# Kernel tuning notes

Measured on AMD Instinct MI355X. Metric: run time of the kernel, lower is better.

## Reference

```python
import jax, jax.numpy as jnp
import numpy as np
from jax import lax

D_MODEL, D_INNER, N_STATE, DT_RANK, K = 1024, 2048, 16, 64, 3
B_SZ, SEQ = 2, 1024

def silu(v):
    return v * jax.nn.sigmoid(v)

def setup_inputs() -> dict:
    key = jax.random.key(0)
    ks = jax.random.split(key, 12)
    s = 0.02
    return {
        'x': jax.random.normal(ks[0], (B_SZ, SEQ, D_MODEL), jnp.float32),
        'A_log': jax.random.normal(ks[1], (D_INNER, N_STATE), jnp.float32) * 0.5,
        'W_in': jax.random.normal(ks[2], (D_MODEL, 2 * D_INNER), jnp.float32) * s,
        'b_in': jax.random.normal(ks[3], (2 * D_INNER,), jnp.float32) * s,
        'conv_w': jax.random.normal(ks[4], (D_INNER, 1, K), jnp.float32) * s,  # depthwise [O,I/g,K]
        'conv_b': jax.random.normal(ks[5], (D_INNER,), jnp.float32) * s,
        'W_x': jax.random.normal(ks[6], (D_INNER, DT_RANK + 2 * N_STATE), jnp.float32) * s,
        'W_dt': jax.random.normal(ks[7], (DT_RANK, D_INNER), jnp.float32) * s,
        'b_dt': jax.random.normal(ks[8], (D_INNER,), jnp.float32) * s,
        'W_out': jax.random.normal(ks[9], (D_INNER, D_MODEL), jnp.float32) * s,
        'b_out': jax.random.normal(ks[10], (D_MODEL,), jnp.float32) * s,
    }

def selective_scan(u, delta, A, B, C):
    # u, delta: [b,l,d]; A: [d,n]; B, C: [b,l,n]
    deltaA = jnp.exp(jnp.einsum('bld,dn->bldn', delta, A))          # [b,l,d,n]
    deltaBu = jnp.einsum('bld,bln,bld->bldn', delta, B, u)           # [b,l,d,n]
    h0 = jnp.zeros((u.shape[0], u.shape[2], A.shape[1]), u.dtype)    # [b,d,n]
    def step(h, inp):
        dA_t, dBu_t, C_t = inp
        h = dA_t * h + dBu_t
        y = jnp.einsum('bdn,bn->bd', h, C_t)
        return h, y
    xs = (jnp.moveaxis(deltaA, 1, 0), jnp.moveaxis(deltaBu, 1, 0), jnp.moveaxis(C, 1, 0))
    _, ys = lax.scan(step, h0, xs)                                   # [l,b,d]
    return jnp.moveaxis(ys, 0, 1)                                    # [b,l,d]

def reference(x, A_log, W_in, b_in, conv_w, conv_b, W_x, W_dt, b_dt, W_out, b_out):
    xr = x @ W_in + b_in                                             # [b,l,2*d_inner]
    u, res = jnp.split(xr, 2, axis=-1)
    # causal depthwise conv1d (pad left k-1, truncate == torch pad=k-1 then slice)
    uc = lax.conv_general_dilated(
        jnp.moveaxis(u, 1, 2), conv_w, window_strides=(1,),
        padding=[(K - 1, 0)], feature_group_count=D_INNER,
        dimension_numbers=('NCH', 'OIH', 'NCH'))
    u = silu(jnp.moveaxis(uc, 2, 1) + conv_b)                        # [b,l,d_inner]
    xp = u @ W_x                                                     # [b,l,dt_rank+2n]
    dt, Bm, Cm = jnp.split(xp, [DT_RANK, DT_RANK + N_STATE], axis=-1)
    delta = jax.nn.softplus(dt @ W_dt + b_dt)                        # [b,l,d_inner]
    A = -jnp.exp(A_log)                                              # [d_inner,n]
    y = selective_scan(u, delta, A, Bm, Cm)                          # [b,l,d_inner]
    y = y * silu(res)
    return y @ W_out + b_out
```

## Files before the change

### kernel.cpp

```cpp
#include <hip/hip_runtime.h>

#define D_MODEL 1024
#define D_INNER 2048
#define N_ST    16
#define DT_RANK 64
#define BSZ     2
#define SEQL    1024
#define NTOK    (BSZ*SEQL)
#define NC      32
#define LC      (SEQL/NC)

typedef __attribute__((ext_vector_type(4))) float f32x4;
typedef __attribute__((ext_vector_type(8))) short bf16x8;

__device__ __forceinline__ short f2b(float f) {
  unsigned u = __builtin_bit_cast(unsigned, f);
  u += 0x7fffu + ((u >> 16) & 1u);
  return (short)(u >> 16);
}

__device__ __forceinline__ float b2f(unsigned short s) {
  return __builtin_bit_cast(float, (unsigned)s << 16);
}

__device__ __forceinline__ void gload16(const void* g, void* l) {
  __builtin_amdgcn_global_load_lds(
      (const __attribute__((address_space(1))) void*)g,
      (__attribute__((address_space(3))) void*)l, 16, 0, 0);
}

template<int SOFTPLUS, int PARTIAL, int RESSPLIT, int OUTB16, int FIXUP>
__global__ __launch_bounds__(256)
void gemm_kernel(const short* __restrict__ A, const short* __restrict__ Bm,
                 const float* __restrict__ bias, float* __restrict__ C,
                 short* __restrict__ upb, short* __restrict__ resb,
                 const float* __restrict__ cw, const float* __restrict__ cb,
                 short* __restrict__ ubuf,
                 int M, int N, int K, int lda, int ldb, int ldc, int kChunk)
{
  __shared__ short sA[2][128 * 64];
  __shared__ short sB[2][128 * 64];
  const int tid  = threadIdx.x;
  const int lane = tid & 63;
  const int wave = tid >> 6;
  const int wr = wave >> 1, wc = wave & 1;
  const int lr = lane & 15, lg = lane >> 4;

  int bx = blockIdx.x, by = blockIdx.y;
  if (RESSPLIT) {
    const int lin = by * 32 + bx;
    const int lb = (lin & 7) * 64 + (lin >> 3);
    bx = lb >> 4; by = lb & 15;
  }
  const int m0 = by * 128;
  const int n0 = bx * 128;
  const int kStart = blockIdx.z * kChunk;
  int kEnd = kStart + kChunk; if (kEnd > K) kEnd = K;
  const int nt = (kEnd - kStart) >> 6;

  if (FIXUP) {
    const int tt = m0 + (tid >> 7);
    const int dd = kStart + (tid & 127);
    const int l  = tt & (SEQL - 1);
    float u2 = b2f((unsigned short)upb[(size_t)tt * 2048 + dd]);
    float u1 = (l >= 1) ? b2f((unsigned short)upb[(size_t)(tt - 1) * 2048 + dd]) : 0.f;
    float u0 = (l >= 2) ? b2f((unsigned short)upb[(size_t)(tt - 2) * 2048 + dd]) : 0.f;
    float r = cb[dd] + cw[dd * 3] * u0 + cw[dd * 3 + 1] * u1 + cw[dd * 3 + 2] * u2;
    ubuf[(size_t)tt * 2048 + dd] = f2b(r / (1.f + __expf(-r)));
    asm volatile("s_waitcnt vmcnt(0)" ::: "memory");
    __syncthreads();
  }

  const int srow = lane >> 3;
  const int scol = ((lane & 7) ^ srow) * 8;
  const short* aS = A + (size_t)(m0 + wave * 32 + srow) * lda + scol + kStart;
  const short* bS = Bm + (size_t)(n0 + wave * 32 + srow) * ldb + scol + kStart;
  const int ldsOff = wave * 2048;

#define STAGE(buf, koff)                                                   \
  {                                                                        \
    _Pragma("unroll")                                                      \
    for (int i_ = 0; i_ < 4; ++i_) {                                       \
      gload16(aS + (size_t)(i_ * 8) * lda + (koff), &sA[buf][ldsOff + i_ * 512]); \
      gload16(bS + (size_t)(i_ * 8) * ldb + (koff), &sB[buf][ldsOff + i_ * 512]); \
    }                                                                      \
  }

  f32x4 acc[4][4];
#pragma unroll
  for (int i = 0; i < 4; ++i)
#pragma unroll
    for (int j = 0; j < 4; ++j) acc[i][j] = (f32x4){0.f, 0.f, 0.f, 0.f};

  STAGE(0, 0);

  for (int t = 0; t < nt; ++t) {
    const int cur = t & 1;
    if (t + 1 < nt) {
      STAGE(cur ^ 1, (t + 1) * 64);
      asm volatile("s_waitcnt vmcnt(8)" ::: "memory");
    } else {
      asm volatile("s_waitcnt vmcnt(0)" ::: "memory");
    }
    __builtin_amdgcn_s_barrier();

#pragma unroll
    for (int kk = 0; kk < 2; ++kk) {
      bf16x8 aF[4], bF[4];
#pragma unroll
      for (int mi = 0; mi < 4; ++mi) {
        const int row = wr * 64 + mi * 16 + lr;
        aF[mi] = *reinterpret_cast<const bf16x8*>(
            &sA[cur][row * 64 + (((kk * 4 + lg) ^ (lr & 7)) * 8)]);
      }
#pragma unroll
      for (int ni = 0; ni < 4; ++ni) {
        const int row = wc * 64 + ni * 16 + lr;
        bF[ni] = *reinterpret_cast<const bf16x8*>(
            &sB[cur][row * 64 + (((kk * 4 + lg) ^ (lr & 7)) * 8)]);
      }
#pragma unroll
      for (int mi = 0; mi < 4; ++mi)
#pragma unroll
        for (int ni = 0; ni < 4; ++ni)
          acc[mi][ni] = __builtin_amdgcn_mfma_f32_16x16x32_bf16(
              aF[mi], bF[ni], acc[mi][ni], 0, 0, 0);
    }
    __builtin_amdgcn_s_barrier();
  }
#undef STAGE

  if (RESSPLIT) {
    if (n0 < 2048) {
      short (*sU)[128] = reinterpret_cast<short (*)[128]>(&sA[0][0]);
#pragma unroll
      for (int mi = 0; mi < 4; ++mi) {
#pragma unroll
        for (int ni = 0; ni < 4; ++ni) {
          const int cl = wc * 64 + ni * 16 + lr;
          const float bv = bias[n0 + cl];
#pragma unroll
          for (int j = 0; j < 4; ++j) {
            const int rl = wr * 64 + mi * 16 + lg * 4 + j;
            const short s = f2b(acc[mi][ni][j] + bv);
            sU[rl][cl] = s;
            if (rl < 2 || rl >= 126)
              upb[(size_t)(m0 + rl) * 2048 + (n0 + cl)] = s;
          }
        }
      }
      __syncthreads();
#pragma unroll
      for (int ni = 0; ni < 4; ++ni) {
        const int cl = wc * 64 + ni * 16 + lr;
        const int col = n0 + cl;
        const float w0 = cw[col * 3], w1 = cw[col * 3 + 1], w2 = cw[col * 3 + 2];
        const float cbv = cb[col];
#pragma unroll
        for (int mi = 0; mi < 4; ++mi) {
#pragma unroll
          for (int j = 0; j < 4; ++j) {
            const int rl = wr * 64 + mi * 16 + lg * 4 + j;
            if (rl >= 2) {
              float r = cbv + w0 * b2f((unsigned short)sU[rl - 2][cl])
                            + w1 * b2f((unsigned short)sU[rl - 1][cl])
                            + w2 * b2f((unsigned short)sU[rl][cl]);
              ubuf[(size_t)(m0 + rl) * 2048 + col] = f2b(r / (1.f + __expf(-r)));
            }
          }
        }
      }
    } else {
#pragma unroll
      for (int mi = 0; mi < 4; ++mi) {
        const int row = m0 + wr * 64 + mi * 16 + lg * 4;
#pragma unroll
        for (int ni = 0; ni < 4; ++ni) {
          const int col = n0 + wc * 64 + ni * 16 + lr;
          const float bv = bias[col];
#pragma unroll
          for (int j = 0; j < 4; ++j) {
            float v = acc[mi][ni][j] + bv;
            resb[(size_t)(row + j) * 2048 + (col - 2048)] =
                f2b(v / (1.f + __expf(-v)));
          }
        }
      }
    }
    return;
  }

#pragma unroll
  for (int mi = 0; mi < 4; ++mi) {
    const int row = m0 + wr * 64 + mi * 16 + lg * 4;
#pragma unroll
    for (int ni = 0; ni < 4; ++ni) {
      const int col = n0 + wc * 64 + ni * 16 + lr;
      if (OUTB16) {
        const float bv = bias[col];
#pragma unroll
        for (int j = 0; j < 4; ++j) {
          float v = acc[mi][ni][j] + bv;
          if (SOFTPLUS) v = fmaxf(v, 0.f) + log1pf(__expf(-fabsf(v)));
          upb[(size_t)(row + j) * ldc + col] = f2b(v);
        }
      } else if (PARTIAL == 2) {
        short* Cs = (short*)C + (size_t)blockIdx.z * M * ldc;
#pragma unroll
        for (int j = 0; j < 4; ++j)
          Cs[(size_t)(row + j) * ldc + col] = f2b(acc[mi][ni][j]);
      } else if (col < N) {
        float* Cp = PARTIAL ? C + (size_t)blockIdx.z * M * ldc : C;
        float bv = (bias != nullptr && blockIdx.z == 0) ? bias[col] : 0.f;
#pragma unroll
        for (int j = 0; j < 4; ++j) {
          float v = acc[mi][ni][j] + bv;
          if (SOFTPLUS) v = fmaxf(v, 0.f) + log1pf(__expf(-fabsf(v)));
          Cp[(size_t)(row + j) * ldc + col] = v;
        }
      }
    }
  }
}

__device__ __forceinline__ void trans_body(const float* __restrict__ in,
                                           short* __restrict__ out,
                                           int R, int C, int bx, int by,
                                           short (*t)[33], int tidx)
{
  const int c0 = bx * 32, r0 = by * 32;
  const int cc = tidx & 31, rr = tidx >> 5;
#pragma unroll
  for (int i = 0; i < 4; ++i)
    t[rr + i * 8][cc] = f2b(in[(size_t)(r0 + rr + i * 8) * C + c0 + cc]);
  __syncthreads();
#pragma unroll
  for (int i = 0; i < 4; ++i)
    out[(size_t)(c0 + rr + i * 8) * R + r0 + cc] = t[cc][rr + i * 8];
}

#define PB_CAST  2048
#define PB_WIN   4096
#define PB_WX    192
#define PB_WDT   128
#define PB_WOUT  2048

__global__ __launch_bounds__(256)
void prep_kernel(const float* __restrict__ x,    const float* __restrict__ W_in,
                 const float* __restrict__ W_x,  const float* __restrict__ W_dt,
                 const float* __restrict__ W_out,
                 short* __restrict__ xb,  short* __restrict__ Wib,
                 short* __restrict__ Wxb, short* __restrict__ Wdtb,
                 short* __restrict__ Wob)
{
  __shared__ short t[32][33];
  const int bid = blockIdx.x, tidx = threadIdx.x;
  if (bid < PB_CAST) {
    const int i = bid * 256 + tidx;
    float4 v = *reinterpret_cast<const float4*>(x + (size_t)i * 4);
    *reinterpret_cast<short4*>(xb + (size_t)i * 4) =
        make_short4(f2b(v.x), f2b(v.y), f2b(v.z), f2b(v.w));
  } else if (bid < PB_CAST + PB_WIN) {
    const int b = bid - PB_CAST;
    trans_body(W_in, Wib, 1024, 4096, b % 128, b / 128, t, tidx);
  } else if (bid < PB_CAST + PB_WIN + PB_WX) {
    const int b = bid - PB_CAST - PB_WIN;
    trans_body(W_x, Wxb, 2048, 96, b % 3, b / 3, t, tidx);
  } else if (bid < PB_CAST + PB_WIN + PB_WX + PB_WDT) {
    const int b = bid - PB_CAST - PB_WIN - PB_WX;
    trans_body(W_dt, Wdtb, 64, 2048, b % 64, b / 64, t, tidx);
  } else {
    const int b = bid - PB_CAST - PB_WIN - PB_WX - PB_WDT;
    trans_body(W_out, Wob, 2048, 1024, b % 32, b / 32, t, tidx);
  }
}

__global__ __launch_bounds__(256)
void combine16_kernel(const float* __restrict__ part, float* __restrict__ xp,
                      short* __restrict__ dtb)
{
  const int gid = blockIdx.x * 256 + threadIdx.x;
  const int r = gid / 24, q = gid - r * 24;
  float4 s = make_float4(0.f, 0.f, 0.f, 0.f);
#pragma unroll
  for (int c = 0; c < 16; ++c) {
    const float4 v = *reinterpret_cast<const float4*>(
        part + (size_t)c * 2048 * 96 + (size_t)r * 96 + q * 4);
    s.x += v.x; s.y += v.y; s.z += v.z; s.w += v.w;
  }
  *reinterpret_cast<float4*>(xp + (size_t)r * 96 + q * 4) = s;
  if (q < 16)
    *reinterpret_cast<short4*>(dtb + (size_t)r * 64 + q * 4) =
        make_short4(f2b(s.x), f2b(s.y), f2b(s.z), f2b(s.w));
}

__global__ __launch_bounds__(256)
void combine4_kernel(const unsigned short* __restrict__ part,
                     const float* __restrict__ bias, float* __restrict__ out)
{
  const int gid = blockIdx.x * 256 + threadIdx.x;
  const int r = gid >> 8, c4 = gid & 255;
  const float4 bv = *reinterpret_cast<const float4*>(bias + c4 * 4);
  float4 s = bv;
#pragma unroll
  for (int z = 0; z < 4; ++z) {
    const ushort4 v = *reinterpret_cast<const ushort4*>(
        part + (size_t)z * 2048 * 1024 + (size_t)r * 1024 + c4 * 4);
    s.x += b2f(v.x); s.y += b2f(v.y); s.z += b2f(v.z); s.w += b2f(v.w);
  }
  *reinterpret_cast<float4*>(out + (size_t)r * 1024 + c4 * 4) = s;
}

__global__ __launch_bounds__(256, 4)
void scan_pass1(const unsigned short* __restrict__ deltab, const unsigned short* __restrict__ ub,
                const float* __restrict__ xp, const float* __restrict__ A_log,
                float* __restrict__ sdl, float* __restrict__ HS)
{
  const int d = blockIdx.y * 256 + threadIdx.x;
  const int c = blockIdx.x, b = blockIdx.z;
  const int t0 = (b << 10) + c * LC;
  float Ac[16];
#pragma unroll
  for (int q = 0; q < 4; ++q) {
    float4 a = *reinterpret_cast<const float4*>(A_log + (size_t)d * 16 + q * 4);
    Ac[q * 4 + 0] = -__expf(a.x); Ac[q * 4 + 1] = -__expf(a.y);
    Ac[q * 4 + 2] = -__expf(a.z); Ac[q * 4 + 3] = -__expf(a.w);
  }
  float h[16];
#pragma unroll
  for (int n = 0; n < 16; ++n) h[n] = 0.f;
  float sd = 0.f;
  const unsigned short* dp = deltab + (size_t)t0 * 2048 + d;
  const unsigned short* up = ub + (size_t)t0 * 2048 + d;
  const float* xb = xp + (size_t)t0 * 96 + DT_RANK;
#pragma unroll 4
  for (int t = 0; t < LC; ++t) {
    float dl = b2f(dp[(size_t)t * 2048]);
    float ul = b2f(up[(size_t)t * 2048]);
    float Bf[16];
#pragma unroll
    for (int q = 0; q < 4; ++q)
      *reinterpret_cast<float4*>(&Bf[q * 4]) =
          *reinterpret_cast<const float4*>(xb + (size_t)t * 96 + q * 4);
    float dlu = dl * ul;
    sd += dl;
#pragma unroll
    for (int n = 0; n < 16; ++n)
      h[n] = __expf(dl * Ac[n]) * h[n] + dlu * Bf[n];
  }
  sdl[((size_t)b * NC + c) * 2048 + d] = sd;
  float* hs = HS + (((size_t)b * NC + c) * 2048 + d) * 16;
#pragma unroll
  for (int q = 0; q < 4; ++q)
    *reinterpret_cast<float4*>(hs + q * 4) =
        make_float4(h[q * 4], h[q * 4 + 1], h[q * 4 + 2], h[q * 4 + 3]);
}

__global__ __launch_bounds__(256)
void scan_pass2(const float* __restrict__ sdl, const float* __restrict__ A_log,
                float* __restrict__ HS)
{
  const int gid = blockIdx.x * 256 + threadIdx.x;
  const int b = gid >> 15, rest = gid & 32767;
  const int d = rest >> 4;
  const float Ac = -__expf(A_log[rest]);
  float P[NC], S[NC];
#pragma unroll
  for (int c = 0; c < NC; ++c)
    P[c] = sdl[(((size_t)b * NC + c) << 11) + d];
#pragma unroll
  for (int c = 0; c < NC; ++c)
    S[c] = HS[(((size_t)b * NC + c) << 15) + rest];
#pragma unroll
  for (int c = 0; c < NC; ++c)
    P[c] = __expf(P[c] * Ac);
  float h = 0.f;
#pragma unroll
  for (int c = 0; c < NC; ++c) {
    HS[(((size_t)b * NC + c) << 15) + rest] = h;
    h = P[c] * h + S[c];
  }
}

__global__ __launch_bounds__(256, 4)
void scan_pass3(const unsigned short* __restrict__ deltab, const unsigned short* __restrict__ ub,
                const float* __restrict__ xp, const float* __restrict__ A_log,
                const float* __restrict__ HS, const unsigned short* __restrict__ rb,
                short* __restrict__ zb)
{
  const int d = blockIdx.y * 256 + threadIdx.x;
  const int c = blockIdx.x, b = blockIdx.z;
  const int t0 = (b << 10) + c * LC;
  float Ac[16];
#pragma unroll
  for (int q = 0; q < 4; ++q) {
    float4 a = *reinterpret_cast<const float4*>(A_log + (size_t)d * 16 + q * 4);
    Ac[q * 4 + 0] = -__expf(a.x); Ac[q * 4 + 1] = -__expf(a.y);
    Ac[q * 4 + 2] = -__expf(a.z); Ac[q * 4 + 3] = -__expf(a.w);
  }
  float h[16];
  const float* hs = HS + (((size_t)b * NC + c) * 2048 + d) * 16;
#pragma unroll
  for (int q = 0; q < 4; ++q) {
    float4 v = *reinterpret_cast<const float4*>(hs + q * 4);
    h[q * 4 + 0] = v.x; h[q * 4 + 1] = v.y; h[q * 4 + 2] = v.z; h[q * 4 + 3] = v.w;
  }
  const unsigned short* dp = deltab + (size_t)t0 * 2048 + d;
  const unsigned short* up = ub + (size_t)t0 * 2048 + d;
  const float* xb = xp + (size_t)t0 * 96 + DT_RANK;
  const float* xc = xp + (size_t)t0 * 96 + DT_RANK + N_ST;
  const unsigned short* rp = rb + (size_t)t0 * 2048 + d;
  short* zp = zb + (size_t)t0 * 2048 + d;
#pragma unroll 4
  for (int t = 0; t < LC; ++t) {
    float dl = b2f(dp[(size_t)t * 2048]);
    float ul = b2f(up[(size_t)t * 2048]);
    float rv = b2f(rp[(size_t)t * 2048]);
    float Bf[16], Cf[16];
#pragma unroll
    for (int q = 0; q < 4; ++q) {
      *reinterpret_cast<float4*>(&Bf[q * 4]) =
          *reinterpret_cast<const float4*>(xb + (size_t)t * 96 + q * 4);
      *reinterpret_cast<float4*>(&Cf[q * 4]) =
          *reinterpret_cast<const float4*>(xc + (size_t)t * 96 + q * 4);
    }
    float dlu = dl * ul;
    float p0 = 0.f, p1 = 0.f, p2 = 0.f, p3 = 0.f;
#pragma unroll
    for (int n = 0; n < 16; ++n) {
      h[n] = __expf(dl * Ac[n]) * h[n] + dlu * Bf[n];
      float t2 = h[n] * Cf[n];
      if ((n & 3) == 0) p0 += t2;
      else if ((n & 3) == 1) p1 += t2;
      else if ((n & 3) == 2) p2 += t2;
      else p3 += t2;
    }
    float p = (p0 + p1) + (p2 + p3);
    zp[(size_t)t * 2048] = f2b(p * rv);
  }
}

extern "C" void kernel_launch(void* const* d_in, const int* in_sizes, int n_in,
                              void* d_out, int out_size, void* d_ws, size_t ws_size,
                              hipStream_t stream)
{
  const float* x      = (const float*)d_in[0];
  const float* A_log  = (const float*)d_in[1];
  const float* W_in   = (const float*)d_in[2];
  const float* b_in   = (const float*)d_in[3];
  const float* conv_w = (const float*)d_in[4];
  const float* conv_b = (const float*)d_in[5];
  const float* W_x    = (const float*)d_in[6];
  const float* W_dt   = (const float*)d_in[7];
  const float* b_dt   = (const float*)d_in[8];
  const float* W_out  = (const float*)d_in[9];
  const float* b_out  = (const float*)d_in[10];
  float* out = (float*)d_out;

  char* p = (char*)d_ws;
  short* upb    = (short*)p; p += (size_t)NTOK * 2048 * 2;
  short* rb     = (short*)p; p += (size_t)NTOK * 2048 * 2;
  short* ub     = (short*)p; p += (size_t)NTOK * 2048 * 2;
  float* xp     = (float*)p; p += (size_t)NTOK * 96 * 4;
  short* dtb    = (short*)p; p += (size_t)NTOK * 64 * 2;
  short* deltab = (short*)p; p += (size_t)NTOK * 2048 * 2;
  short* zb     = (short*)p; p += (size_t)NTOK * 2048 * 2;
  short* xb     = (short*)p; p += (size_t)NTOK * 1024 * 2;
  short* Wib    = (short*)p; p += (size_t)4096 * 1024 * 2;
  short* Wxb    = (short*)p; p += (size_t)128 * 2048 * 2;
  short* Wdtb   = (short*)p; p += (size_t)2048 * 64 * 2;
  short* Wob    = (short*)p; p += (size_t)1024 * 2048 * 2;
  char*  scr    = p;         p += (size_t)16 * 1024 * 1024;
  float* xppart = (float*)scr;
  short* opart  = (short*)scr;
  float* sdl    = (float*)p; p += (size_t)BSZ * NC * 2048 * 4;
  float* HS     = (float*)p; p += (size_t)BSZ * NC * 2048 * 16 * 4;

  prep_kernel<<<dim3(PB_CAST + PB_WIN + PB_WX + PB_WDT + PB_WOUT), 256, 0, stream>>>(
      x, W_in, W_x, W_dt, W_out, xb, Wib, Wxb, Wdtb, Wob);

  gemm_kernel<0, 0, 1, 0, 0><<<dim3(32, 16, 1), 256, 0, stream>>>(
      xb, Wib, b_in, nullptr, upb, rb, conv_w, conv_b, ub,
      NTOK, 4096, 1024, 1024, 1024, 0, 1024);
  gemm_kernel<0, 1, 0, 0, 1><<<dim3(1, 16, 16), 256, 0, stream>>>(
      ub, Wxb, nullptr, xppart, upb, nullptr, conv_w, conv_b, ub,
      NTOK, 96, 2048, 2048, 2048, 96, 128);
  combine16_kernel<<<dim3(192), 256, 0, stream>>>(xppart, xp, dtb);
  gemm_kernel<1, 0, 0, 1, 0><<<dim3(16, 16, 1), 256, 0, stream>>>(
      dtb, Wdtb, b_dt, nullptr, deltab, nullptr, nullptr, nullptr, nullptr,
      NTOK, 2048, 64, 64, 64, 2048, 64);
  scan_pass1<<<dim3(NC, 8, BSZ), 256, 0, stream>>>(
      (const unsigned short*)deltab, (const unsigned short*)ub, xp, A_log, sdl, HS);
  scan_pass2<<<dim3(256), 256, 0, stream>>>(sdl, A_log, HS);
  scan_pass3<<<dim3(NC, 8, BSZ), 256, 0, stream>>>(
      (const unsigned short*)deltab, (const unsigned short*)ub, xp, A_log, HS,
      (const unsigned short*)rb, zb);
  gemm_kernel<0, 2, 0, 0, 0><<<dim3(8, 16, 4), 256, 0, stream>>>(
      zb, Wob, nullptr, (float*)opart, nullptr, nullptr, nullptr, nullptr, nullptr,
      NTOK, 1024, 2048, 2048, 2048, 1024, 512);
  combine4_kernel<<<dim3(2048), 256, 0, stream>>>(
      (const unsigned short*)opart, b_out, out);
}
```

Baseline: 143.9 us.

## Fuse x_proj GEMM into in_proj epilogue and fix tile-boundary rows in combine

The in_proj GEMM epilogue now feeds the conv+SiLU output tile (128 tokens × 128 channels) from LDS straight into a small MFMA product with W_x. It writes per-column-block partial sums, which removes the separate split-K x_proj GEMM launch and its reread of the u buffer. The combine kernel gains extra blocks that recompute the two boundary rows per 128-token tile, where the conv needs rows from the previous tile, and compute their x_proj with a scalar dot product. This costs one fewer launch and less traffic, but adds epilogue work, uncached global loads of W_x inside the GEMM, and a serial per-row dot-product path.

After: 174.2 us. 21.0% more time.

```diff
diff --git a/kernel.cpp b/kernel.cpp
--- a/kernel.cpp
+++ b/kernel.cpp
@@ -29,13 +29,13 @@
       (__attribute__((address_space(3))) void*)l, 16, 0, 0);
 }
 
-template<int SOFTPLUS, int PARTIAL, int RESSPLIT, int OUTB16, int FIXUP>
+template<int SOFTPLUS, int PARTIAL, int RESSPLIT, int OUTB16>
 __global__ __launch_bounds__(256)
 void gemm_kernel(const short* __restrict__ A, const short* __restrict__ Bm,
                  const float* __restrict__ bias, float* __restrict__ C,
                  short* __restrict__ upb, short* __restrict__ resb,
                  const float* __restrict__ cw, const float* __restrict__ cb,
-                 short* __restrict__ ubuf,
+                 short* __restrict__ ubuf, const short* __restrict__ Wx,
                  int M, int N, int K, int lda, int ldb, int ldc, int kChunk)
 {
   __shared__ short sA[2][128 * 64];
@@ -58,19 +58,6 @@
   int kEnd = kStart + kChunk; if (kEnd > K) kEnd = K;
   const int nt = (kEnd - kStart) >> 6;
 
-  if (FIXUP) {
-    const int tt = m0 + (tid >> 7);
-    const int dd = kStart + (tid & 127);
-    const int l  = tt & (SEQL - 1);
-    float u2 = b2f((unsigned short)upb[(size_t)tt * 2048 + dd]);
-    float u1 = (l >= 1) ? b2f((unsigned short)upb[(size_t)(tt - 1) * 2048 + dd]) : 0.f;
-    float u0 = (l >= 2) ? b2f((unsigned short)upb[(size_t)(tt - 2) * 2048 + dd]) : 0.f;
-    float r = cb[dd] + cw[dd * 3] * u0 + cw[dd * 3 + 1] * u1 + cw[dd * 3 + 2] * u2;
-    ubuf[(size_t)tt * 2048 + dd] = f2b(r / (1.f + __expf(-r)));
-    asm volatile("s_waitcnt vmcnt(0)" ::: "memory");
-    __syncthreads();
-  }
-
   const int srow = lane >> 3;
   const int scol = ((lane & 7) ^ srow) * 8;
   const short* aS = A + (size_t)(m0 + wave * 32 + srow) * lda + scol + kStart;
@@ -133,6 +120,7 @@
   if (RESSPLIT) {
     if (n0 < 2048) {
       short (*sU)[128] = reinterpret_cast<short (*)[128]>(&sA[0][0]);
+      short* sVp = &sB[0][0];
 #pragma unroll
       for (int mi = 0; mi < 4; ++mi) {
 #pragma unroll
@@ -161,13 +149,54 @@
 #pragma unroll
           for (int j = 0; j < 4; ++j) {
             const int rl = wr * 64 + mi * 16 + lg * 4 + j;
+            short val = 0;
             if (rl >= 2) {
               float r = cbv + w0 * b2f((unsigned short)sU[rl - 2][cl])
                             + w1 * b2f((unsigned short)sU[rl - 1][cl])
                             + w2 * b2f((unsigned short)sU[rl][cl]);
-              ubuf[(size_t)(m0 + rl) * 2048 + col] = f2b(r / (1.f + __expf(-r)));
+              val = f2b(r / (1.f + __expf(-r)));
+              ubuf[(size_t)(m0 + rl) * 2048 + col] = val;
             }
+            sVp[rl * 128 + ((((cl >> 3) ^ (rl & 7)) << 3) | (cl & 7))] = val;
           }
+        }
+      }
+      __syncthreads();
+      f32x4 acc2[2][6];
+#pragma unroll
+      for (int m2 = 0; m2 < 2; ++m2)
+#pragma unroll
+        for (int nf = 0; nf < 6; ++nf) acc2[m2][nf] = (f32x4){0.f, 0.f, 0.f, 0.f};
+#pragma unroll
+      for (int ks = 0; ks < 4; ++ks) {
+        bf16x8 aF2[2], bF2[6];
+#pragma unroll
+        for (int m2 = 0; m2 < 2; ++m2) {
+          const int row = wave * 32 + m2 * 16 + lr;
+          aF2[m2] = *reinterpret_cast<const bf16x8*>(
+              &sVp[row * 128 + (((ks * 4 + lg) ^ (row & 7)) << 3)]);
+        }
+#pragma unroll
+        for (int nf = 0; nf < 6; ++nf)
+          bF2[nf] = *reinterpret_cast<const bf16x8*>(
+              Wx + (size_t)(nf * 16 + lr) * 2048 + n0 + ks * 32 + lg * 8);
+#pragma unroll
+        for (int m2 = 0; m2 < 2; ++m2)
+#pragma unroll
+          for (int nf = 0; nf < 6; ++nf)
+            acc2[m2][nf] = __builtin_amdgcn_mfma_f32_16x16x32_bf16(
+                aF2[m2], bF2[nf], acc2[m2][nf], 0, 0, 0);
+      }
+      float* xpp = C + (size_t)bx * 2048 * 96;
+#pragma unroll
+      for (int m2 = 0; m2 < 2; ++m2) {
+        const int row = m0 + wave * 32 + m2 * 16 + lg * 4;
+#pragma unroll
+        for (int nf = 0; nf < 6; ++nf) {
+          const int o = nf * 16 + lr;
+#pragma unroll
+          for (int j = 0; j < 4; ++j)
+            xpp[(size_t)(row + j) * 96 + o] = acc2[m2][nf][j];
         }
       }
     } else {
@@ -277,21 +306,72 @@
 
 __global__ __launch_bounds__(256)
 void combine16_kernel(const float* __restrict__ part, float* __restrict__ xp,
-                      short* __restrict__ dtb)
-{
-  const int gid = blockIdx.x * 256 + threadIdx.x;
-  const int r = gid / 24, q = gid - r * 24;
-  float4 s = make_float4(0.f, 0.f, 0.f, 0.f);
-#pragma unroll
-  for (int c = 0; c < 16; ++c) {
-    const float4 v = *reinterpret_cast<const float4*>(
-        part + (size_t)c * 2048 * 96 + (size_t)r * 96 + q * 4);
-    s.x += v.x; s.y += v.y; s.z += v.z; s.w += v.w;
-  }
-  *reinterpret_cast<float4*>(xp + (size_t)r * 96 + q * 4) = s;
-  if (q < 16)
-    *reinterpret_cast<short4*>(dtb + (size_t)r * 64 + q * 4) =
-        make_short4(f2b(s.x), f2b(s.y), f2b(s.z), f2b(s.w));
+                      short* __restrict__ dtb, const unsigned short* __restrict__ upb,
+                      const float* __restrict__ cw, const float* __restrict__ cb,
+                      short* __restrict__ ub, const short* __restrict__ Wxb)
+{
+  __shared__ short su[2048];
+  if (blockIdx.x < 192) {
+    const int gid = blockIdx.x * 256 + threadIdx.x;
+    const int r = gid / 24, q = gid - r * 24;
+    if ((r & 127) < 2) return;
+    float4 s = make_float4(0.f, 0.f, 0.f, 0.f);
+#pragma unroll
+    for (int c = 0; c < 16; ++c) {
+      const float4 v = *reinterpret_cast<const float4*>(
+          part + (size_t)c * 2048 * 96 + (size_t)r * 96 + q * 4);
+      s.x += v.x; s.y += v.y; s.z += v.z; s.w += v.w;
+    }
+    *reinterpret_cast<float4*>(xp + (size_t)r * 96 + q * 4) = s;
+    if (q < 16)
+      *reinterpret_cast<short4*>(dtb + (size_t)r * 64 + q * 4) =
+          make_short4(f2b(s.x), f2b(s.y), f2b(s.z), f2b(s.w));
+    return;
+  }
+  const int bb = blockIdx.x - 192;
+  const int t = (bb >> 1) * 128 + (bb & 1);
+  const int l = t & (SEQL - 1);
+  const int d0 = threadIdx.x * 8;
+  ushort4 z4; z4.x = z4.y = z4.z = z4.w = 0;
+  ushort4 c2a = *reinterpret_cast<const ushort4*>(upb + (size_t)t * 2048 + d0);
+  ushort4 c2b = *reinterpret_cast<const ushort4*>(upb + (size_t)t * 2048 + d0 + 4);
+  ushort4 c1a = (l >= 1) ? *reinterpret_cast<const ushort4*>(upb + (size_t)(t - 1) * 2048 + d0) : z4;
+  ushort4 c1b = (l >= 1) ? *reinterpret_cast<const ushort4*>(upb + (size_t)(t - 1) * 2048 + d0 + 4) : z4;
+  ushort4 c0a = (l >= 2) ? *reinterpret_cast<const ushort4*>(upb + (size_t)(t - 2) * 2048 + d0) : z4;
+  ushort4 c0b = (l >= 2) ? *reinterpret_cast<const ushort4*>(upb + (size_t)(t - 2) * 2048 + d0 + 4) : z4;
+  unsigned short u2[8] = {c2a.x, c2a.y, c2a.z, c2a.w, c2b.x, c2b.y, c2b.z, c2b.w};
+  unsigned short u1[8] = {c1a.x, c1a.y, c1a.z, c1a.w, c1b.x, c1b.y, c1b.z, c1b.w};
+  unsigned short u0[8] = {c0a.x, c0a.y, c0a.z, c0a.w, c0b.x, c0b.y, c0b.z, c0b.w};
+  short outv[8];
+#pragma unroll
+  for (int e = 0; e < 8; ++e) {
+    const int dd = d0 + e;
+    float r = cb[dd] + cw[dd * 3] * b2f(u0[e]) + cw[dd * 3 + 1] * b2f(u1[e])
+                     + cw[dd * 3 + 2] * b2f(u2[e]);
+    outv[e] = f2b(r / (1.f + __expf(-r)));
+    su[dd] = outv[e];
+  }
+  *reinterpret_cast<short4*>(ub + (size_t)t * 2048 + d0) =
+      make_short4(outv[0], outv[1], outv[2], outv[3]);
+  *reinterpret_cast<short4*>(ub + (size_t)t * 2048 + d0 + 4) =
+      make_short4(outv[4], outv[5], outv[6], outv[7]);
+  __syncthreads();
+  const int w = threadIdx.x >> 6, ln = threadIdx.x & 63;
+  for (int i = 0; i < 24; ++i) {
+    const int o = w * 24 + i;
+    float s = 0.f;
+#pragma unroll 8
+    for (int j = 0; j < 32; ++j) {
+      const int d = ln + 64 * j;
+      s += b2f((unsigned short)su[d]) * b2f((unsigned short)Wxb[(size_t)o * 2048 + d]);
+    }
+    s += __shfl_xor(s, 32); s += __shfl_xor(s, 16); s += __shfl_xor(s, 8);
+    s += __shfl_xor(s, 4);  s += __shfl_xor(s, 2);  s += __shfl_xor(s, 1);
+    if (ln == 0) {
+      xp[(size_t)t * 96 + o] = s;
+      if (o < 64) dtb[(size_t)t * 64 + o] = f2b(s);
+    }
+  }
 }
 
 __global__ __launch_bounds__(256)
@@ -479,15 +559,13 @@
   prep_kernel<<<dim3(PB_CAST + PB_WIN + PB_WX + PB_WDT + PB_WOUT), 256, 0, stream>>>(
       x, W_in, W_x, W_dt, W_out, xb, Wib, Wxb, Wdtb, Wob);
 
-  gemm_kernel<0, 0, 1, 0, 0><<<dim3(32, 16, 1), 256, 0, stream>>>(
-      xb, Wib, b_in, nullptr, upb, rb, conv_w, conv_b, ub,
+  gemm_kernel<0, 0, 1, 0><<<dim3(32, 16, 1), 256, 0, stream>>>(
+      xb, Wib, b_in, xppart, upb, rb, conv_w, conv_b, ub, Wxb,
       NTOK, 4096, 1024, 1024, 1024, 0, 1024);
-  gemm_kernel<0, 1, 0, 0, 1><<<dim3(1, 16, 16), 256, 0, stream>>>(
-      ub, Wxb, nullptr, xppart, upb, nullptr, conv_w, conv_b, ub,
-      NTOK, 96, 2048, 2048, 2048, 96, 128);
-  combine16_kernel<<<dim3(192), 256, 0, stream>>>(xppart, xp, dtb);
-  gemm_kernel<1, 0, 0, 1, 0><<<dim3(16, 16, 1), 256, 0, stream>>>(
-      dtb, Wdtb, b_dt, nullptr, deltab, nullptr, nullptr, nullptr, nullptr,
+  combine16_kernel<<<dim3(224), 256, 0, stream>>>(
+      xppart, xp, dtb, (const unsigned short*)upb, conv_w, conv_b, ub, Wxb);
+  gemm_kernel<1, 0, 0, 1><<<dim3(16, 16, 1), 256, 0, stream>>>(
+      dtb, Wdtb, b_dt, nullptr, deltab, nullptr, nullptr, nullptr, nullptr, nullptr,
       NTOK, 2048, 64, 64, 64, 2048, 64);
   scan_pass1<<<dim3(NC, 8, BSZ), 256, 0, stream>>>(
       (const unsigned short*)deltab, (const unsigned short*)ub, xp, A_log, sdl, HS);
@@ -495,8 +573,8 @@
   scan_pass3<<<dim3(NC, 8, BSZ), 256, 0, stream>>>(
       (const unsigned short*)deltab, (const unsigned short*)ub, xp, A_log, HS,
       (const unsigned short*)rb, zb);
-  gemm_kernel<0, 2, 0, 0, 0><<<dim3(8, 16, 4), 256, 0, stream>>>(
-      zb, Wob, nullptr, (float*)opart, nullptr, nullptr, nullptr, nullptr, nullptr,
+  gemm_kernel<0, 2, 0, 0><<<dim3(8, 16, 4), 256, 0, stream>>>(
+      zb, Wob, nullptr, (float*)opart, nullptr, nullptr, nullptr, nullptr, nullptr, nullptr,
       NTOK, 1024, 2048, 2048, 2048, 1024, 512);
   combine4_kernel<<<dim3(2048), 256, 0, stream>>>(
       (const unsigned short*)opart, b_out, out);
```
